# Kernel optimization log

Hardware: AMD Instinct MI355X
Metric: run time of the kernel (lower is better)

The kernel has to match this reference:

```python
import jax, jax.numpy as jnp
import numpy as np

N_KERNELS = 5
MUL_FACTOR = 2.0
# 2.0 ** (arange(5) - 2) = [0.25, 0.5, 1, 2, 4]
BANDWIDTH_MULTIPLIERS = MUL_FACTOR ** (np.arange(N_KERNELS) - N_KERNELS // 2)


def setup_inputs() -> dict:
    key = jax.random.key(0)
    kx, ky = jax.random.split(key)
    X = jax.random.normal(kx, (4096, 256), dtype=jnp.float32)
    Y = jax.random.normal(ky, (4096, 256), dtype=jnp.float32)
    return {"X": X, "Y": Y}


def _pairwise_sq_dists(Z):
    # ||z_i - z_j||^2 via GEMM; clamp tiny negatives from roundoff.
    sq = jnp.sum(Z * Z, axis=-1)  # [2N]
    d2 = sq[:, None] + sq[None, :] - 2.0 * (Z @ Z.T)  # [2N, 2N]
    return jnp.maximum(d2, 0.0)


def reference(X, Y):
    n = X.shape[0]
    Z = jnp.concatenate([X, Y], axis=0)  # [2N, D]
    d2 = _pairwise_sq_dists(Z)  # [2N, 2N]
    n_samples = d2.shape[0]
    # bandwidth uses .data in torch -> detached
    bandwidth = jax.lax.stop_gradient(d2.sum()) / (n_samples ** 2 - n_samples)
    mults = jnp.asarray(BANDWIDTH_MULTIPLIERS, dtype=d2.dtype)  # [5]
    # K = sum_k exp(-d2 / (bandwidth * mult_k))
    K = jnp.exp(-d2[None, :, :] / (bandwidth * mults)[:, None, None]).sum(axis=0)
    XX = K[:n, :n].mean()
    XY = K[:n, n:].mean()
    YY = K[n:, n:].mean()
    return XX - 2.0 * XY + YY
```

## Files before the change

kernel.cpp:

```cpp
#include <hip/hip_runtime.h>
#include <math.h>


#define N_HALF 4096
#define DIM 256
#define M_TOT 8192
#define TILE 128
#define NT 64
#define NT_HALF 32
#define NCHUNK 512

typedef unsigned short ushort_t;
typedef __attribute__((ext_vector_type(8))) short short8;
typedef __attribute__((ext_vector_type(4))) float floatx4;

__device__ ushort_t g_zf[M_TOT * DIM];

__device__ __forceinline__ ushort_t f2bf(float f) {
    unsigned u = __float_as_uint(f);
    u += 0x7fffu + ((u >> 16) & 1u);
    return (ushort_t)(u >> 16);
}

__device__ __forceinline__ void gload_lds16(const ushort_t* g, ushort_t* l) {
    __builtin_amdgcn_global_load_lds(
        (const __attribute__((address_space(1))) void*)g,
        (__attribute__((address_space(3))) void*)l, 16, 0, 0);
}

__device__ __forceinline__ void stage1(const ushort_t* gA, const ushort_t* gB,
                                       int kk, ushort_t* buf, int wave, int lane) {
#pragma unroll
    for (int i = 0; i < 2; ++i) {
        const int c = wave * 2 + i;
        gload_lds16(gA + (size_t)c * 4096 + kk * 512 + lane * 8, buf + c * 512);
        gload_lds16(gB + (size_t)c * 4096 + kk * 512 + lane * 8, buf + 4096 + c * 512);
    }
}

__global__ __launch_bounds__(256) void k_prep(const float* __restrict__ X,
                                              const float* __restrict__ Y,
                                              float* __restrict__ sq,
                                              float* __restrict__ colsum_r,
                                              float* __restrict__ Ssum_r) {
    __shared__ float cpart[4][256];
    __shared__ float spart[4];
    const int t = threadIdx.x, wave = t >> 6, lane = t & 63;
    const int row0 = blockIdx.x * 16 + wave * 4;
    const int kk = lane >> 3, q = (lane >> 1) & 3, j0 = (lane & 1) * 4;
    float c0 = 0.f, c1 = 0.f, c2 = 0.f, c3 = 0.f, ssum = 0.f;
#pragma unroll
    for (int i = 0; i < 4; ++i) {
        const int row = row0 + i;
        const float* p = (row < N_HALF) ? (X + (size_t)row * DIM)
                                        : (Y + (size_t)(row - N_HALF) * DIM);
        const float4 v = *((const float4*)p + lane);
        ushort4 hi;
        hi.x = f2bf(v.x); hi.y = f2bf(v.y); hi.z = f2bf(v.z); hi.w = f2bf(v.w);
        const int rb = row >> 4, m = row & 15;
        *(ushort4*)(g_zf + (size_t)rb * 4096 + kk * 512 + q * 128 + m * 8 + j0) = hi;
        c0 += v.x; c1 += v.y; c2 += v.z; c3 += v.w;
        float s = fmaf(v.x, v.x, fmaf(v.y, v.y, fmaf(v.z, v.z, v.w * v.w)));
#pragma unroll
        for (int off = 32; off > 0; off >>= 1) s += __shfl_xor(s, off);
        if (lane == 0) sq[row] = s;
        ssum += s;
    }
    float4 cp; cp.x = c0; cp.y = c1; cp.z = c2; cp.w = c3;
    *(float4*)&cpart[wave][lane * 4] = cp;
    if (lane == 0) spart[wave] = ssum;
    __syncthreads();
    const float cs = cpart[0][t] + cpart[1][t] + cpart[2][t] + cpart[3][t];
    const int rep = blockIdx.x & 7;
    atomicAdd(&colsum_r[rep * 256 + t], cs);
    if (t == 0) atomicAdd(&Ssum_r[rep], spart[0] + spart[1] + spart[2] + spart[3]);
}

__global__ __launch_bounds__(256) void k_bw(const float* __restrict__ colsum_r,
                                            const float* __restrict__ Ssum_r,
                                            float* __restrict__ c2out) {
    __shared__ double sred[4];
    const int t = threadIdx.x, lane = t & 63, wave = t >> 6;
    float csf = 0.f;
#pragma unroll
    for (int r = 0; r < 8; ++r) csf += colsum_r[r * 256 + t];
    double p = (double)csf * (double)csf;
#pragma unroll
    for (int off = 32; off > 0; off >>= 1) p += __shfl_xor(p, off);
    if (lane == 0) sred[wave] = p;
    __syncthreads();
    if (t == 0) {
        const double SS = sred[0] + sred[1] + sred[2] + sred[3];
        float Sf = 0.f;
#pragma unroll
        for (int r = 0; r < 8; ++r) Sf += Ssum_r[r];
        const double sum_d2 = 2.0 * (double)M_TOT * (double)Sf - 2.0 * SS;
        const double bw = sum_d2 / ((double)M_TOT * (double)M_TOT - (double)M_TOT);
        c2out[0] = (float)(1.4426950408889634 / (4.0 * bw));
    }
}

__global__ __launch_bounds__(256, 2) void k_gram(const float* __restrict__ sq,
                                                 const float* __restrict__ c2p,
                                                 double* __restrict__ acc,
                                                 unsigned* __restrict__ cnt,
                                                 float* __restrict__ out) {
    __shared__ __attribute__((aligned(16))) ushort_t lds[4][8192];
    __shared__ double redw[4][3];

    const int bid = (int)blockIdx.x;
    const int cc = (bid & 7) * 64 + (bid >> 3);
    const int nst = ((cc & 15) == 0) ? 5 : 4;
    const int f0 = cc * 4 + ((cc + 15) >> 4);

    const int t = threadIdx.x;
    const int lane = t & 63, wave = t >> 6;
    const int l15 = lane & 15, quad = lane >> 4;
    const int wrow = (wave >> 1) * 64, wcol = (wave & 1) * 64;
    const int a0 = (wave >> 1) * 4, b0 = (wave & 1) * 4;
    const int laneoff = quad * 128 + l15 * 8;

    const float c2 = c2p[0];
    const float twoc2 = 2.f * c2;

    int ti = (int)((129.0f - sqrtf(16641.0f - 8.0f * (float)f0)) * 0.5f);
    if (ti < 0) ti = 0; if (ti > NT - 1) ti = NT - 1;
    while (ti * NT - ti * (ti - 1) / 2 > f0) --ti;
    while ((ti + 1) * NT - (ti + 1) * ti / 2 <= f0) ++ti;
    int tj = ti + (f0 - (ti * NT - ti * (ti - 1) / 2));

    int s_ti = ti, s_tj = tj, s_kk = 0;
    const ushort_t* sgA = g_zf + (size_t)s_ti * 32768;
    const ushort_t* sgB = g_zf + (size_t)s_tj * 32768;
#define ADV_STAGE() do { if (++s_kk == 8) { s_kk = 0; ++s_tj;                 \
        if (s_tj == NT) { ++s_ti; s_tj = s_ti; }                              \
        sgA = g_zf + (size_t)s_ti * 32768;                                    \
        sgB = g_zf + (size_t)s_tj * 32768; } } while (0)

#pragma unroll
    for (int p = 0; p < 3; ++p) {
        stage1(sgA, sgB, s_kk, lds[p], wave, lane);
        ADV_STAGE();
    }

    double lxx = 0.0, lxy = 0.0, lyy = 0.0;

#pragma unroll 1
    for (int s = 0; s < nst; ++s) {
        const bool last = (s == nst - 1);

        floatx4 accv[4][4];
#pragma unroll
        for (int mi = 0; mi < 4; ++mi)
#pragma unroll
            for (int ni = 0; ni < 4; ++ni) accv[mi][ni] = (floatx4)0.f;

#pragma unroll
        for (int kkc = 0; kkc < 8; ++kkc) {
            if (last && kkc == 6)      asm volatile("s_waitcnt vmcnt(4)" ::: "memory");
            else if (last && kkc == 7) asm volatile("s_waitcnt vmcnt(0)" ::: "memory");
            else                       asm volatile("s_waitcnt vmcnt(8)" ::: "memory");
            __builtin_amdgcn_s_barrier();
            __builtin_amdgcn_sched_barrier(0);

            const ushort_t* lA = lds[kkc & 3];
            const ushort_t* lB = lds[kkc & 3] + 4096;
            short8 af[4], bf[4];
#pragma unroll
            for (int mi = 0; mi < 4; ++mi)
                af[mi] = *(const short8*)(lA + (a0 + mi) * 512 + laneoff);
#pragma unroll
            for (int ni = 0; ni < 4; ++ni)
                bf[ni] = *(const short8*)(lB + (b0 + ni) * 512 + laneoff);

            if (!last || kkc < 5) {
                stage1(sgA, sgB, s_kk, lds[(kkc + 3) & 3], wave, lane);
                ADV_STAGE();
            }

            __builtin_amdgcn_s_setprio(1);
#pragma unroll
            for (int mi = 0; mi < 4; ++mi)
#pragma unroll
                for (int ni = 0; ni < 4; ++ni)
                    accv[mi][ni] = __builtin_amdgcn_mfma_f32_16x16x32_bf16(
                        af[mi], bf[ni], accv[mi][ni], 0, 0, 0);
            __builtin_amdgcn_s_setprio(0);
        }

        const int arow0 = ti * TILE, brow0 = tj * TILE;
        float nsj[4];
#pragma unroll
        for (int ni = 0; ni < 4; ++ni)
            nsj[ni] = -c2 * sq[brow0 + wcol + ni * 16 + l15];
        floatx4 nsi4[4];
#pragma unroll
        for (int mi = 0; mi < 4; ++mi) {
            const float4 sv = *(const float4*)&sq[arow0 + wrow + mi * 16 + quad * 4];
            nsi4[mi][0] = -c2 * sv.x; nsi4[mi][1] = -c2 * sv.y;
            nsi4[mi][2] = -c2 * sv.z; nsi4[mi][3] = -c2 * sv.w;
        }
        floatx4 sum4 = (floatx4)0.f;
#pragma unroll
        for (int mi = 0; mi < 4; ++mi) {
#pragma unroll
            for (int ni = 0; ni < 4; ++ni) {
                const floatx4 addv = nsi4[mi] + (floatx4)nsj[ni];
                floatx4 arg = twoc2 * accv[mi][ni] + addv;
                floatx4 tt;
#pragma unroll
                for (int r = 0; r < 4; ++r) tt[r] = exp2f(fminf(arg[r], 0.f));
                const floatx4 t2 = tt * tt, t4 = t2 * t2, t8 = t4 * t4, t16 = t8 * t8;
                sum4 += (tt + t2) + (t4 + t8) + t16;
            }
        }
        const float fsum = (sum4[0] + sum4[1]) + (sum4[2] + sum4[3]);
        const double contrib = ((ti == tj) ? 1.0 : 2.0) * (double)fsum;
        if (tj < NT_HALF)       lxx += contrib;
        else if (ti < NT_HALF)  lxy += contrib;
        else                    lyy += contrib;

        ++tj; if (tj == NT) { ++ti; tj = ti; }
    }
#undef ADV_STAGE

#pragma unroll
    for (int off = 32; off > 0; off >>= 1) {
        lxx += __shfl_xor(lxx, off);
        lxy += __shfl_xor(lxy, off);
        lyy += __shfl_xor(lyy, off);
    }
    if (lane == 0) { redw[wave][0] = lxx; redw[wave][1] = lxy; redw[wave][2] = lyy; }
    __syncthreads();
    if (t == 0) {
        double sxx = 0.0, sxy = 0.0, syy = 0.0;
#pragma unroll
        for (int wv = 0; wv < 4; ++wv) {
            sxx += redw[wv][0]; sxy += redw[wv][1]; syy += redw[wv][2];
        }
        if (sxx != 0.0) atomicAdd(&acc[0], sxx);
        if (sxy != 0.0) atomicAdd(&acc[1], sxy);
        if (syy != 0.0) atomicAdd(&acc[2], syy);
        __threadfence();
        const unsigned old = atomicAdd(cnt, 1u);
        if (old == (0xAAAAAAAAu + (unsigned)(NCHUNK - 1)) ||
            old == (unsigned)(NCHUNK - 1)) {
            const double xx = atomicAdd(&acc[0], 0.0);
            const double xy = atomicAdd(&acc[1], 0.0);
            const double yy = atomicAdd(&acc[2], 0.0);
            out[0] = (float)((xx + yy - xy) *
                             (1.0 / ((double)N_HALF * (double)N_HALF)));
        }
    }
}

extern "C" void kernel_launch(void* const* d_in, const int* in_sizes, int n_in,
                              void* d_out, int out_size, void* d_ws, size_t ws_size,
                              hipStream_t stream) {
    const float* X = (const float*)d_in[0];
    const float* Y = (const float*)d_in[1];
    char* ws = (char*)d_ws;
    float* sq        = (float*)ws;
    float* colsum_r  = (float*)(ws + 32768);
    float* Ssum_r    = (float*)(ws + 40960);
    unsigned* cnt    = (unsigned*)(ws + 40992);
    double* acc      = (double*)(ws + 41000);
    float* c2ws      = (float*)(ws + 41024);
    float* out = (float*)d_out;

    hipLaunchKernelGGL(k_prep, dim3(512), dim3(256), 0, stream,
                       X, Y, sq, colsum_r, Ssum_r);
    hipLaunchKernelGGL(k_bw, dim3(1), dim3(256), 0, stream,
                       colsum_r, Ssum_r, c2ws);
    hipLaunchKernelGGL(k_gram, dim3(NCHUNK), dim3(256), 0, stream,
                       sq, c2ws, acc, cnt, out);
}
```

Measured before the change: 113.8 us.

## Fuse prep, bandwidth and gram kernels into one kernel with atomic grid sync

Merges the three launches (row prep and bf16 packing, bandwidth reduction, gram/MMD accumulation) into one kernel. Blocks first grab prep chunks from an atomic ticket counter. The last block to finish computes the bandwidth constant and publishes it through a ready flag, while the other blocks spin-wait on that flag before starting the gram phase. This removes two kernel launches and their inter-kernel gaps. In exchange it relies on all 512 blocks being co-resident to avoid deadlock, and on the workspace counters starting zeroed or 0xAA-poisoned each call.

```diff
diff --git a/kernel.cpp b/kernel.cpp
--- a/kernel.cpp
+++ b/kernel.cpp
@@ -9,6 +9,8 @@
 #define NT 64
 #define NT_HALF 32
 #define NCHUNK 512
+#define NPCHUNK 512
+#define MAGIC 0x13371337u
 
 typedef unsigned short ushort_t;
 typedef __attribute__((ext_vector_type(8))) short short8;
@@ -38,89 +40,124 @@
     }
 }
 
-__global__ __launch_bounds__(256) void k_prep(const float* __restrict__ X,
-                                              const float* __restrict__ Y,
-                                              float* __restrict__ sq,
-                                              float* __restrict__ colsum_r,
-                                              float* __restrict__ Ssum_r) {
-    __shared__ float cpart[4][256];
-    __shared__ float spart[4];
-    const int t = threadIdx.x, wave = t >> 6, lane = t & 63;
-    const int row0 = blockIdx.x * 16 + wave * 4;
-    const int kk = lane >> 3, q = (lane >> 1) & 3, j0 = (lane & 1) * 4;
-    float c0 = 0.f, c1 = 0.f, c2 = 0.f, c3 = 0.f, ssum = 0.f;
-#pragma unroll
-    for (int i = 0; i < 4; ++i) {
-        const int row = row0 + i;
-        const float* p = (row < N_HALF) ? (X + (size_t)row * DIM)
-                                        : (Y + (size_t)(row - N_HALF) * DIM);
-        const float4 v = *((const float4*)p + lane);
-        ushort4 hi;
-        hi.x = f2bf(v.x); hi.y = f2bf(v.y); hi.z = f2bf(v.z); hi.w = f2bf(v.w);
-        const int rb = row >> 4, m = row & 15;
-        *(ushort4*)(g_zf + (size_t)rb * 4096 + kk * 512 + q * 128 + m * 8 + j0) = hi;
-        c0 += v.x; c1 += v.y; c2 += v.z; c3 += v.w;
-        float s = fmaf(v.x, v.x, fmaf(v.y, v.y, fmaf(v.z, v.z, v.w * v.w)));
-#pragma unroll
-        for (int off = 32; off > 0; off >>= 1) s += __shfl_xor(s, off);
-        if (lane == 0) sq[row] = s;
-        ssum += s;
-    }
-    float4 cp; cp.x = c0; cp.y = c1; cp.z = c2; cp.w = c3;
-    *(float4*)&cpart[wave][lane * 4] = cp;
-    if (lane == 0) spart[wave] = ssum;
-    __syncthreads();
-    const float cs = cpart[0][t] + cpart[1][t] + cpart[2][t] + cpart[3][t];
-    const int rep = blockIdx.x & 7;
-    atomicAdd(&colsum_r[rep * 256 + t], cs);
-    if (t == 0) atomicAdd(&Ssum_r[rep], spart[0] + spart[1] + spart[2] + spart[3]);
-}
-
-__global__ __launch_bounds__(256) void k_bw(const float* __restrict__ colsum_r,
-                                            const float* __restrict__ Ssum_r,
-                                            float* __restrict__ c2out) {
-    __shared__ double sred[4];
-    const int t = threadIdx.x, lane = t & 63, wave = t >> 6;
-    float csf = 0.f;
-#pragma unroll
-    for (int r = 0; r < 8; ++r) csf += colsum_r[r * 256 + t];
-    double p = (double)csf * (double)csf;
-#pragma unroll
-    for (int off = 32; off > 0; off >>= 1) p += __shfl_xor(p, off);
-    if (lane == 0) sred[wave] = p;
-    __syncthreads();
-    if (t == 0) {
-        const double SS = sred[0] + sred[1] + sred[2] + sred[3];
-        float Sf = 0.f;
-#pragma unroll
-        for (int r = 0; r < 8; ++r) Sf += Ssum_r[r];
-        const double sum_d2 = 2.0 * (double)M_TOT * (double)Sf - 2.0 * SS;
-        const double bw = sum_d2 / ((double)M_TOT * (double)M_TOT - (double)M_TOT);
-        c2out[0] = (float)(1.4426950408889634 / (4.0 * bw));
-    }
-}
-
-__global__ __launch_bounds__(256, 2) void k_gram(const float* __restrict__ sq,
-                                                 const float* __restrict__ c2p,
-                                                 double* __restrict__ acc,
-                                                 unsigned* __restrict__ cnt,
-                                                 float* __restrict__ out) {
+__device__ __forceinline__ unsigned norm_cnt(unsigned raw) {
+    return (raw >= 0xAAAAAAAAu) ? raw - 0xAAAAAAAAu : raw;
+}
+
+__global__ __launch_bounds__(256, 2) void k_all(
+        const float* __restrict__ X, const float* __restrict__ Y,
+        float* __restrict__ sq, float* __restrict__ colsum_r,
+        float* __restrict__ Ssum_r, unsigned* __restrict__ tkt,
+        unsigned* __restrict__ done, unsigned* __restrict__ ready,
+        float* __restrict__ c2ws, double* __restrict__ acc,
+        unsigned* __restrict__ cnt, float* __restrict__ out) {
     __shared__ __attribute__((aligned(16))) ushort_t lds[4][8192];
     __shared__ double redw[4][3];
+    __shared__ int sh_chunk, sh_fin;
+    __shared__ float sh_c2;
+
+    const int t = threadIdx.x;
+    const int lane = t & 63, wave = t >> 6;
+
+    {
+        float* cpart = (float*)&lds[0][0];
+        float* spart = (float*)&lds[1][0];
+        double* sred = (double*)&lds[2][0];
+        const int kk = lane >> 3, q = (lane >> 1) & 3, j0 = (lane & 1) * 4;
+        for (;;) {
+            if (t == 0) {
+                const unsigned nm = norm_cnt(atomicAdd(tkt, 1u));
+                sh_chunk = (nm < (unsigned)NPCHUNK) ? (int)nm : -1;
+            }
+            __syncthreads();
+            const int chunk = sh_chunk;
+            if (chunk < 0) break;
+            const int row0 = chunk * 16 + wave * 4;
+            float s0 = 0.f, s1 = 0.f, s2 = 0.f, s3 = 0.f, ssum = 0.f;
+#pragma unroll
+            for (int i = 0; i < 4; ++i) {
+                const int row = row0 + i;
+                const float* p = (row < N_HALF)
+                                     ? (X + (size_t)row * DIM)
+                                     : (Y + (size_t)(row - N_HALF) * DIM);
+                const float4 v = *((const float4*)p + lane);
+                ushort4 hi;
+                hi.x = f2bf(v.x); hi.y = f2bf(v.y);
+                hi.z = f2bf(v.z); hi.w = f2bf(v.w);
+                const int rb = row >> 4, m = row & 15;
+                *(ushort4*)(g_zf + (size_t)rb * 4096 + kk * 512 + q * 128 +
+                            m * 8 + j0) = hi;
+                s0 += v.x; s1 += v.y; s2 += v.z; s3 += v.w;
+                float s = fmaf(v.x, v.x,
+                               fmaf(v.y, v.y, fmaf(v.z, v.z, v.w * v.w)));
+#pragma unroll
+                for (int off = 32; off > 0; off >>= 1) s += __shfl_xor(s, off);
+                if (lane == 0) sq[row] = s;
+                ssum += s;
+            }
+            float4 cp; cp.x = s0; cp.y = s1; cp.z = s2; cp.w = s3;
+            *(float4*)&cpart[wave * 256 + lane * 4] = cp;
+            if (lane == 0) spart[wave] = ssum;
+            __syncthreads();
+            const float cs = cpart[t] + cpart[256 + t] + cpart[512 + t] +
+                             cpart[768 + t];
+            const int rep = chunk & 7;
+            atomicAdd(&colsum_r[rep * 256 + t], cs);
+            if (t == 0) {
+                atomicAdd(&Ssum_r[rep],
+                          spart[0] + spart[1] + spart[2] + spart[3]);
+                __threadfence();
+                sh_fin = (norm_cnt(atomicAdd(done, 1u)) ==
+                          (unsigned)(NPCHUNK - 1));
+            }
+            __syncthreads();
+            if (sh_fin) {
+                float csf = 0.f;
+#pragma unroll
+                for (int r = 0; r < 8; ++r)
+                    csf += atomicAdd(&colsum_r[r * 256 + t], 0.f);
+                double p = (double)csf * (double)csf;
+#pragma unroll
+                for (int off = 32; off > 0; off >>= 1) p += __shfl_xor(p, off);
+                if (lane == 0) sred[wave] = p;
+                __syncthreads();
+                if (t == 0) {
+                    const double SS = sred[0] + sred[1] + sred[2] + sred[3];
+                    float Sf = 0.f;
+#pragma unroll
+                    for (int r = 0; r < 8; ++r)
+                        Sf += atomicAdd(&Ssum_r[r], 0.f);
+                    const double sum_d2 =
+                        2.0 * (double)M_TOT * (double)Sf - 2.0 * SS;
+                    const double bw = sum_d2 / ((double)M_TOT * (double)M_TOT -
+                                                (double)M_TOT);
+                    c2ws[0] = (float)(1.4426950408889634 / (4.0 * bw));
+                    __threadfence();
+                    atomicExch(ready, MAGIC);
+                }
+            }
+            __syncthreads();
+        }
+    }
+
+    if (t == 0) {
+        while (atomicAdd(ready, 0u) != MAGIC) __builtin_amdgcn_s_sleep(2);
+        sh_c2 = atomicAdd(c2ws, 0.0f);
+    }
+    __syncthreads();
+    __threadfence();
 
     const int bid = (int)blockIdx.x;
     const int cc = (bid & 7) * 64 + (bid >> 3);
     const int nst = ((cc & 15) == 0) ? 5 : 4;
     const int f0 = cc * 4 + ((cc + 15) >> 4);
 
-    const int t = threadIdx.x;
-    const int lane = t & 63, wave = t >> 6;
     const int l15 = lane & 15, quad = lane >> 4;
     const int wrow = (wave >> 1) * 64, wcol = (wave & 1) * 64;
     const int a0 = (wave >> 1) * 4, b0 = (wave & 1) * 4;
     const int laneoff = quad * 128 + l15 * 8;
 
-    const float c2 = c2p[0];
+    const float c2 = sh_c2;
     const float twoc2 = 2.f * c2;
 
     int ti = (int)((129.0f - sqrtf(16641.0f - 8.0f * (float)f0)) * 0.5f);
@@ -243,8 +280,7 @@
         if (syy != 0.0) atomicAdd(&acc[2], syy);
         __threadfence();
         const unsigned old = atomicAdd(cnt, 1u);
-        if (old == (0xAAAAAAAAu + (unsigned)(NCHUNK - 1)) ||
-            old == (unsigned)(NCHUNK - 1)) {
+        if (norm_cnt(old) == (unsigned)(NCHUNK - 1)) {
             const double xx = atomicAdd(&acc[0], 0.0);
             const double xy = atomicAdd(&acc[1], 0.0);
             const double yy = atomicAdd(&acc[2], 0.0);
@@ -266,12 +302,12 @@
     unsigned* cnt    = (unsigned*)(ws + 40992);
     double* acc      = (double*)(ws + 41000);
     float* c2ws      = (float*)(ws + 41024);
+    unsigned* tkt    = (unsigned*)(ws + 41028);
+    unsigned* done   = (unsigned*)(ws + 41032);
+    unsigned* ready  = (unsigned*)(ws + 41036);
     float* out = (float*)d_out;
 
-    hipLaunchKernelGGL(k_prep, dim3(512), dim3(256), 0, stream,
-                       X, Y, sq, colsum_r, Ssum_r);
-    hipLaunchKernelGGL(k_bw, dim3(1), dim3(256), 0, stream,
-                       colsum_r, Ssum_r, c2ws);
-    hipLaunchKernelGGL(k_gram, dim3(NCHUNK), dim3(256), 0, stream,
-                       sq, c2ws, acc, cnt, out);
-}
+    hipLaunchKernelGGL(k_all, dim3(NCHUNK), dim3(256), 0, stream,
+                       X, Y, sq, colsum_r, Ssum_r, tkt, done, ready,
+                       c2ws, acc, cnt, out);
+}
```

Result: slower. 220.4 us (+93.6%).
